# Optimization experiments

Hardware: AMD Instinct MI355X
Metric: run time of the kernel (lower is better)

The kernel has to match this reference:

```python
import jax, jax.numpy as jnp
import numpy as np

NUM_EMBEDDINGS = 512
EMBEDDING_DIM = 128
COMMITMENT_COST = 0.6
MID_HR = 100.0
HR_RANGE = 70.0


def setup_inputs() -> dict:
    key = jax.random.key(0)
    k1, k2 = jax.random.split(key)
    inputs = jax.random.normal(k1, (64, 2048, EMBEDDING_DIM), dtype=jnp.float32)
    # torch init: uniform(-1/K, 1/K)
    emb_weight = jax.random.uniform(
        k2, (NUM_EMBEDDINGS, EMBEDDING_DIM), dtype=jnp.float32,
        minval=-1.0 / NUM_EMBEDDINGS, maxval=1.0 / NUM_EMBEDDINGS)
    scaling = jnp.ones((NUM_EMBEDDINGS,), dtype=jnp.float32)
    return {"inputs": inputs, "emb_weight": emb_weight, "scaling": scaling}


def reference(inputs, emb_weight, scaling):
    B, T, D = inputs.shape
    K = emb_weight.shape[0]
    flat = inputs.reshape(-1, D)  # [N, D]
    # squared L2 distances to all codes: [N, K]
    distances = (
        jnp.sum(flat * flat, axis=1, keepdims=True)
        + jnp.sum(emb_weight * emb_weight, axis=1)
        - 2.0 * flat @ emb_weight.T
    )
    hr_values = jnp.linspace(40.0, 180.0, K, dtype=jnp.float32)
    hr_weights = 1.0 + scaling * ((hr_values - MID_HR) / HR_RANGE)  # [K]
    encoding_indices = jnp.argmin(distances * hr_weights[None, :], axis=1)  # [N]
    # one-hot @ codebook == direct gather
    quantized = emb_weight[encoding_indices].reshape(inputs.shape)
    e_latent_loss = jnp.mean((jax.lax.stop_gradient(quantized) - inputs) ** 2)
    q_latent_loss = jnp.mean((quantized - jax.lax.stop_gradient(inputs)) ** 2)
    loss = q_latent_loss + COMMITMENT_COST * e_latent_loss
    # straight-through estimator
    quantized_st = inputs + jax.lax.stop_gradient(quantized - inputs)
    return quantized_st, loss, encoding_indices.reshape(B, T)
```

## Files before the change

kernel.cpp:

```cpp
#include <hip/hip_runtime.h>

#define NCODES 512
#define DIM 128
#define NROWS (64*2048)
#define QN (NROWS*DIM)
#define BLK_ROWS 256
#define NBLOCKS (NROWS/BLK_ROWS)
#define NWAVES 8

typedef __attribute__((ext_vector_type(4))) float f32x4;

#define GLOAD_LDS16(gp, lp) __builtin_amdgcn_global_load_lds( \
    (__attribute__((address_space(1))) void*)(gp), \
    (__attribute__((address_space(3))) void*)(lp), 16, 0, 0)

__global__ void vq_prep(const float* __restrict__ emb, const float* __restrict__ scaling,
                        unsigned char* __restrict__ e8frag,
                        float* __restrict__ wv, float* __restrict__ wse,
                        float* __restrict__ wrcp) {
  int k = blockIdx.x;
  int l = threadIdx.x;
  float2 v = ((const float2*)(emb + k * DIM))[l];
  float ss = v.x * v.x + v.y * v.y;
#pragma unroll
  for (int m = 1; m < 64; m <<= 1) ss += __shfl_xor(ss, m);
  int p = __builtin_amdgcn_cvt_pk_fp8_f32(v.x * 512.0f, v.y * 512.0f, 0, false);
  int t = k >> 4, col = k & 15;
  int c = l >> 4, g = (l >> 2) & 3, jp = l & 3;
  *(unsigned short*)(e8frag + (((t * 4 + c) * 64 + g * 16 + col) << 3) + 2 * jp) =
      (unsigned short)(p & 0xFFFF);
  if (l == 0) {
    float hr = 40.0f + (float)k * (140.0f / 511.0f);
    float wt = 1.0f + scaling[k] * ((hr - 100.0f) * (1.0f / 70.0f));
    wv[k] = wt;
    wse[k] = wt * ss;
    wrcp[k] = 1.0f / wt;
  }
}

struct SmemT {
  unsigned char frag[NCODES * DIM];
  float w[NCODES];
  float wse[NCODES];
  float wrcp[NCODES];
  float lossp[NWAVES];
};

__global__ __launch_bounds__(512, 4) void vq_main(
    const float* __restrict__ x,
    const float* __restrict__ emb32,
    const unsigned char* __restrict__ e8frag,
    const float* __restrict__ wv,
    const float* __restrict__ wse,
    const float* __restrict__ wrcp,
    float* __restrict__ out_q,
    float* __restrict__ out_idx,
    float* __restrict__ out_loss) {
  __shared__ SmemT sm;
  const int tid = threadIdx.x;
  const int wave = tid >> 6, lane = tid & 63;
  const int g = lane >> 4, lr = lane & 15;
  const long rowbase = (long)blockIdx.x * BLK_ROWS + wave * 32;

  float4 xv[2][4][2];
#pragma unroll
  for (int rg = 0; rg < 2; rg++) {
    const float* xr = x + (rowbase + rg * 16 + lr) * DIM + g * 8;
#pragma unroll
    for (int c = 0; c < 4; c++) {
      xv[rg][c][0] = *(const float4*)(xr + c * 32);
      xv[rg][c][1] = *(const float4*)(xr + c * 32 + 4);
    }
  }

  {
#pragma unroll
    for (int i = 0; i < 8; i++) {
      int slot = i * 512 + tid;
      GLOAD_LDS16(e8frag + slot * 16, sm.frag + slot * 16);
    }
    sm.w[tid] = wv[tid]; sm.wse[tid] = wse[tid]; sm.wrcp[tid] = wrcp[tid];
    int t2 = tid + 512 - 512; (void)t2;
  }

  long a[2][4];
  float sr[2][4];
  {
    float srow[2];
#pragma unroll
    for (int rg = 0; rg < 2; rg++) {
      float ss = 0.f;
#pragma unroll
      for (int c = 0; c < 4; c++) {
        float4 v0 = xv[rg][c][0];
        float4 v1 = xv[rg][c][1];
        ss += v0.x * v0.x + v0.y * v0.y + v0.z * v0.z + v0.w * v0.w;
        ss += v1.x * v1.x + v1.y * v1.y + v1.z * v1.z + v1.w * v1.w;
        int lo = __builtin_amdgcn_cvt_pk_fp8_f32(v0.x, v0.y, 0, false);
        lo = __builtin_amdgcn_cvt_pk_fp8_f32(v0.z, v0.w, lo, true);
        int hi = __builtin_amdgcn_cvt_pk_fp8_f32(v1.x, v1.y, 0, false);
        hi = __builtin_amdgcn_cvt_pk_fp8_f32(v1.z, v1.w, hi, true);
        a[rg][c] = (long)(((unsigned long long)(unsigned)hi << 32) |
                          (unsigned long long)(unsigned)lo);
      }
      ss += __shfl_xor(ss, 16);
      ss += __shfl_xor(ss, 32);
      srow[rg] = ss;
    }
#pragma unroll
    for (int rg = 0; rg < 2; rg++)
#pragma unroll
      for (int r = 0; r < 4; r++)
        sr[rg][r] = __shfl(srow[rg], g * 4 + r);
  }
  __syncthreads();

  unsigned pmin[2][4];
#pragma unroll
  for (int rg = 0; rg < 2; rg++)
#pragma unroll
    for (int r = 0; r < 4; r++) pmin[rg][r] = 0xFFFFFFFFu;

  const long* __restrict__ bbase = (const long*)sm.frag + lane;
#pragma unroll 2
  for (int t = 0; t < 32; t++) {
    const unsigned code = t * 16 + lr;
    const float wt = sm.w[code];
    const float bb = sm.wse[code];
    const float m2w = -2.0f * wt * (1.0f / 512.0f);
    f32x4 acc0 = {0.f, 0.f, 0.f, 0.f};
    f32x4 acc1 = {0.f, 0.f, 0.f, 0.f};
#pragma unroll
    for (int c = 0; c < 4; c++) {
      long bf = bbase[(t * 4 + c) * 64];
      acc0 = __builtin_amdgcn_mfma_f32_16x16x32_fp8_fp8(a[0][c], bf, acc0, 0, 0, 0);
      acc1 = __builtin_amdgcn_mfma_f32_16x16x32_fp8_fp8(a[1][c], bf, acc1, 0, 0, 0);
    }
#pragma unroll
    for (int r = 0; r < 4; r++) {
      float v0 = fmaf(m2w, acc0[r], fmaf(wt, sr[0][r], bb));
      float v1 = fmaf(m2w, acc1[r], fmaf(wt, sr[1][r], bb));
      unsigned u0 = (__builtin_bit_cast(unsigned, v0) & 0xFFFFFE00u) | code;
      unsigned u1 = (__builtin_bit_cast(unsigned, v1) & 0xFFFFFE00u) | code;
      pmin[0][r] = min(pmin[0][r], u0);
      pmin[1][r] = min(pmin[1][r], u1);
    }
  }

#pragma unroll
  for (int m = 1; m <= 8; m <<= 1) {
#pragma unroll
    for (int rg = 0; rg < 2; rg++)
#pragma unroll
      for (int r = 0; r < 4; r++) {
        unsigned o = (unsigned)__shfl_xor((int)pmin[rg][r], m);
        pmin[rg][r] = min(pmin[rg][r], o);
      }
  }

  const uint4* __restrict__ esrc = (const uint4*)emb32;
  uint4* __restrict__ outu = (uint4*)out_q + rowbase * 32;
  const int col = lane & 31;
  const int hi2 = lane >> 5;
  int scode[16];
#pragma unroll
  for (int it = 0; it < 16; it++) {
    const int row0 = 2 * it;
    const int rg = row0 >> 4;
    const int gn = (row0 >> 2) & 3;
    const int r0 = row0 & 3;
    int c0 = __shfl((int)pmin[rg][r0], gn * 16);
    int c1 = __shfl((int)pmin[rg][r0 + 1], gn * 16);
    scode[it] = (hi2 ? c1 : c0) & 511;
  }

  uint4 vbuf[8];
#pragma unroll
  for (int j = 0; j < 8; j++)
    vbuf[j] = esrc[scode[j] * 32 + col];

  {
    float l0 = 0.f;
#pragma unroll
    for (int rg = 0; rg < 2; rg++)
#pragma unroll
      for (int r = 0; r < 4; r++) {
        unsigned wn = pmin[rg][r];
        int ci = (int)(wn & 511u);
        float dist = __builtin_bit_cast(float, wn & 0xFFFFFE00u);
        l0 = fmaf(dist, sm.wrcp[ci], l0);
        if (lr == 0) out_idx[rowbase + rg * 16 + g * 4 + r] = (float)ci;
      }
    l0 += __shfl_xor(l0, 16);
    l0 += __shfl_xor(l0, 32);
    if (lane == 0) sm.lossp[wave] = l0;
  }

#pragma unroll
  for (int j = 0; j < 8; j++)
    outu[j * 64 + lane] = vbuf[j];
#pragma unroll
  for (int j = 0; j < 8; j++)
    vbuf[j] = esrc[scode[8 + j] * 32 + col];
#pragma unroll
  for (int j = 0; j < 8; j++)
    outu[(8 + j) * 64 + lane] = vbuf[j];

  __syncthreads();
  if (wave == 0 && lane < NWAVES) {
    float s = sm.lossp[lane];
#pragma unroll
    for (int m = 1; m < NWAVES; m <<= 1) s += __shfl_xor(s, m);
    if (lane == 0) atomicAdd(out_loss, s * (1.6f / (float)QN));
  }
}

extern "C" void kernel_launch(void* const* d_in, const int* in_sizes, int n_in,
                              void* d_out, int out_size, void* d_ws, size_t ws_size,
                              hipStream_t stream) {
  const float* x = (const float*)d_in[0];
  const float* emb = (const float*)d_in[1];
  const float* scaling = (const float*)d_in[2];

  float* out_q = (float*)d_out;
  float* out_loss = out_q + QN;
  float* out_idx = out_q + QN + 1;

  unsigned char* e8frag = (unsigned char*)d_ws;
  float* wv = (float*)((char*)d_ws + NCODES * DIM);
  float* wse = wv + NCODES;
  float* wrcp = wse + NCODES;

  hipMemsetAsync(out_loss, 0, sizeof(float), stream);
  vq_prep<<<NCODES, 64, 0, stream>>>(emb, scaling, e8frag, wv, wse, wrcp);
  vq_main<<<NBLOCKS, 512, 0, stream>>>(x, emb, e8frag, wv, wse, wrcp,
                                       out_q, out_idx, out_loss);
}
```

Before: 43.02 us.

## Halve rows per block: one 16-row MFMA tile per wave instead of two

```diff
diff --git a/kernel.cpp b/kernel.cpp
--- a/kernel.cpp
+++ b/kernel.cpp
@@ -4,7 +4,7 @@
 #define DIM 128
 #define NROWS (64*2048)
 #define QN (NROWS*DIM)
-#define BLK_ROWS 256
+#define BLK_ROWS 128
 #define NBLOCKS (NROWS/BLK_ROWS)
 #define NWAVES 8
 
@@ -60,16 +60,15 @@
   const int tid = threadIdx.x;
   const int wave = tid >> 6, lane = tid & 63;
   const int g = lane >> 4, lr = lane & 15;
-  const long rowbase = (long)blockIdx.x * BLK_ROWS + wave * 32;
-
-  float4 xv[2][4][2];
-#pragma unroll
-  for (int rg = 0; rg < 2; rg++) {
-    const float* xr = x + (rowbase + rg * 16 + lr) * DIM + g * 8;
+  const long rowbase = (long)blockIdx.x * BLK_ROWS + wave * 16;
+
+  float4 xv[4][2];
+  {
+    const float* xr = x + (rowbase + lr) * DIM + g * 8;
 #pragma unroll
     for (int c = 0; c < 4; c++) {
-      xv[rg][c][0] = *(const float4*)(xr + c * 32);
-      xv[rg][c][1] = *(const float4*)(xr + c * 32 + 4);
+      xv[c][0] = *(const float4*)(xr + c * 32);
+      xv[c][1] = *(const float4*)(xr + c * 32 + 4);
     }
   }
 
@@ -80,46 +79,36 @@
       GLOAD_LDS16(e8frag + slot * 16, sm.frag + slot * 16);
     }
     sm.w[tid] = wv[tid]; sm.wse[tid] = wse[tid]; sm.wrcp[tid] = wrcp[tid];
-    int t2 = tid + 512 - 512; (void)t2;
-  }
-
-  long a[2][4];
-  float sr[2][4];
-  {
-    float srow[2];
-#pragma unroll
-    for (int rg = 0; rg < 2; rg++) {
-      float ss = 0.f;
-#pragma unroll
-      for (int c = 0; c < 4; c++) {
-        float4 v0 = xv[rg][c][0];
-        float4 v1 = xv[rg][c][1];
-        ss += v0.x * v0.x + v0.y * v0.y + v0.z * v0.z + v0.w * v0.w;
-        ss += v1.x * v1.x + v1.y * v1.y + v1.z * v1.z + v1.w * v1.w;
-        int lo = __builtin_amdgcn_cvt_pk_fp8_f32(v0.x, v0.y, 0, false);
-        lo = __builtin_amdgcn_cvt_pk_fp8_f32(v0.z, v0.w, lo, true);
-        int hi = __builtin_amdgcn_cvt_pk_fp8_f32(v1.x, v1.y, 0, false);
-        hi = __builtin_amdgcn_cvt_pk_fp8_f32(v1.z, v1.w, hi, true);
-        a[rg][c] = (long)(((unsigned long long)(unsigned)hi << 32) |
-                          (unsigned long long)(unsigned)lo);
-      }
-      ss += __shfl_xor(ss, 16);
-      ss += __shfl_xor(ss, 32);
-      srow[rg] = ss;
-    }
-#pragma unroll
-    for (int rg = 0; rg < 2; rg++)
-#pragma unroll
-      for (int r = 0; r < 4; r++)
-        sr[rg][r] = __shfl(srow[rg], g * 4 + r);
+  }
+
+  long a[4];
+  float sr[4];
+  {
+    float ss = 0.f;
+#pragma unroll
+    for (int c = 0; c < 4; c++) {
+      float4 v0 = xv[c][0];
+      float4 v1 = xv[c][1];
+      ss += v0.x * v0.x + v0.y * v0.y + v0.z * v0.z + v0.w * v0.w;
+      ss += v1.x * v1.x + v1.y * v1.y + v1.z * v1.z + v1.w * v1.w;
+      int lo = __builtin_amdgcn_cvt_pk_fp8_f32(v0.x, v0.y, 0, false);
+      lo = __builtin_amdgcn_cvt_pk_fp8_f32(v0.z, v0.w, lo, true);
+      int hi = __builtin_amdgcn_cvt_pk_fp8_f32(v1.x, v1.y, 0, false);
+      hi = __builtin_amdgcn_cvt_pk_fp8_f32(v1.z, v1.w, hi, true);
+      a[c] = (long)(((unsigned long long)(unsigned)hi << 32) |
+                    (unsigned long long)(unsigned)lo);
+    }
+    ss += __shfl_xor(ss, 16);
+    ss += __shfl_xor(ss, 32);
+#pragma unroll
+    for (int r = 0; r < 4; r++)
+      sr[r] = __shfl(ss, g * 4 + r);
   }
   __syncthreads();
 
-  unsigned pmin[2][4];
-#pragma unroll
-  for (int rg = 0; rg < 2; rg++)
-#pragma unroll
-    for (int r = 0; r < 4; r++) pmin[rg][r] = 0xFFFFFFFFu;
+  unsigned pmin[4];
+#pragma unroll
+  for (int r = 0; r < 4; r++) pmin[r] = 0xFFFFFFFFu;
 
   const long* __restrict__ bbase = (const long*)sm.frag + lane;
 #pragma unroll 2
@@ -128,49 +117,39 @@
     const float wt = sm.w[code];
     const float bb = sm.wse[code];
     const float m2w = -2.0f * wt * (1.0f / 512.0f);
-    f32x4 acc0 = {0.f, 0.f, 0.f, 0.f};
-    f32x4 acc1 = {0.f, 0.f, 0.f, 0.f};
+    f32x4 acc = {0.f, 0.f, 0.f, 0.f};
 #pragma unroll
     for (int c = 0; c < 4; c++) {
       long bf = bbase[(t * 4 + c) * 64];
-      acc0 = __builtin_amdgcn_mfma_f32_16x16x32_fp8_fp8(a[0][c], bf, acc0, 0, 0, 0);
-      acc1 = __builtin_amdgcn_mfma_f32_16x16x32_fp8_fp8(a[1][c], bf, acc1, 0, 0, 0);
+      acc = __builtin_amdgcn_mfma_f32_16x16x32_fp8_fp8(a[c], bf, acc, 0, 0, 0);
     }
 #pragma unroll
     for (int r = 0; r < 4; r++) {
-      float v0 = fmaf(m2w, acc0[r], fmaf(wt, sr[0][r], bb));
-      float v1 = fmaf(m2w, acc1[r], fmaf(wt, sr[1][r], bb));
-      unsigned u0 = (__builtin_bit_cast(unsigned, v0) & 0xFFFFFE00u) | code;
-      unsigned u1 = (__builtin_bit_cast(unsigned, v1) & 0xFFFFFE00u) | code;
-      pmin[0][r] = min(pmin[0][r], u0);
-      pmin[1][r] = min(pmin[1][r], u1);
+      float v = fmaf(m2w, acc[r], fmaf(wt, sr[r], bb));
+      unsigned u = (__builtin_bit_cast(unsigned, v) & 0xFFFFFE00u) | code;
+      pmin[r] = min(pmin[r], u);
     }
   }
 
 #pragma unroll
   for (int m = 1; m <= 8; m <<= 1) {
 #pragma unroll
-    for (int rg = 0; rg < 2; rg++)
-#pragma unroll
-      for (int r = 0; r < 4; r++) {
-        unsigned o = (unsigned)__shfl_xor((int)pmin[rg][r], m);
-        pmin[rg][r] = min(pmin[rg][r], o);
-      }
+    for (int r = 0; r < 4; r++) {
+      unsigned o = (unsigned)__shfl_xor((int)pmin[r], m);
+      pmin[r] = min(pmin[r], o);
+    }
   }
 
   const uint4* __restrict__ esrc = (const uint4*)emb32;
   uint4* __restrict__ outu = (uint4*)out_q + rowbase * 32;
   const int col = lane & 31;
   const int hi2 = lane >> 5;
-  int scode[16];
-#pragma unroll
-  for (int it = 0; it < 16; it++) {
+  int scode[8];
+#pragma unroll
+  for (int it = 0; it < 8; it++) {
     const int row0 = 2 * it;
-    const int rg = row0 >> 4;
-    const int gn = (row0 >> 2) & 3;
-    const int r0 = row0 & 3;
-    int c0 = __shfl((int)pmin[rg][r0], gn * 16);
-    int c1 = __shfl((int)pmin[rg][r0 + 1], gn * 16);
+    int c0 = __shfl((int)pmin[row0 & 3], (row0 >> 2) * 16);
+    int c1 = __shfl((int)pmin[(row0 + 1) & 3], ((row0 + 1) >> 2) * 16);
     scode[it] = (hi2 ? c1 : c0) & 511;
   }
 
@@ -182,15 +161,13 @@
   {
     float l0 = 0.f;
 #pragma unroll
-    for (int rg = 0; rg < 2; rg++)
-#pragma unroll
-      for (int r = 0; r < 4; r++) {
-        unsigned wn = pmin[rg][r];
-        int ci = (int)(wn & 511u);
-        float dist = __builtin_bit_cast(float, wn & 0xFFFFFE00u);
-        l0 = fmaf(dist, sm.wrcp[ci], l0);
-        if (lr == 0) out_idx[rowbase + rg * 16 + g * 4 + r] = (float)ci;
-      }
+    for (int r = 0; r < 4; r++) {
+      unsigned wn = pmin[r];
+      int ci = (int)(wn & 511u);
+      float dist = __builtin_bit_cast(float, wn & 0xFFFFFE00u);
+      l0 = fmaf(dist, sm.wrcp[ci], l0);
+      if (lr == 0) out_idx[rowbase + g * 4 + r] = (float)ci;
+    }
     l0 += __shfl_xor(l0, 16);
     l0 += __shfl_xor(l0, 32);
     if (lane == 0) sm.lossp[wave] = l0;
@@ -199,12 +176,6 @@
 #pragma unroll
   for (int j = 0; j < 8; j++)
     outu[j * 64 + lane] = vbuf[j];
-#pragma unroll
-  for (int j = 0; j < 8; j++)
-    vbuf[j] = esrc[scode[8 + j] * 32 + col];
-#pragma unroll
-  for (int j = 0; j < 8; j++)
-    outu[(8 + j) * 64 + lane] = vbuf[j];
 
   __syncthreads();
   if (wave == 0 && lane < NWAVES) {
```

Measured after the change: 44.75 us. 1.04x slower.

## Replace FP8 MFMA distance search with norm-bound pruning and exact fallback

Applied to the files above, without the earlier changes.

```diff
diff --git a/kernel.cpp b/kernel.cpp
--- a/kernel.cpp
+++ b/kernel.cpp
@@ -8,51 +8,40 @@
 #define NBLOCKS (NROWS/BLK_ROWS)
 #define NWAVES 8
 
-typedef __attribute__((ext_vector_type(4))) float f32x4;
-
-#define GLOAD_LDS16(gp, lp) __builtin_amdgcn_global_load_lds( \
-    (__attribute__((address_space(1))) void*)(gp), \
-    (__attribute__((address_space(3))) void*)(lp), 16, 0, 0)
-
 __global__ void vq_prep(const float* __restrict__ emb, const float* __restrict__ scaling,
-                        unsigned char* __restrict__ e8frag,
-                        float* __restrict__ wv, float* __restrict__ wse,
-                        float* __restrict__ wrcp) {
+                        float* __restrict__ wv, float* __restrict__ ssv,
+                        float* __restrict__ betav, float* __restrict__ gammav) {
   int k = blockIdx.x;
   int l = threadIdx.x;
   float2 v = ((const float2*)(emb + k * DIM))[l];
   float ss = v.x * v.x + v.y * v.y;
 #pragma unroll
   for (int m = 1; m < 64; m <<= 1) ss += __shfl_xor(ss, m);
-  int p = __builtin_amdgcn_cvt_pk_fp8_f32(v.x * 512.0f, v.y * 512.0f, 0, false);
-  int t = k >> 4, col = k & 15;
-  int c = l >> 4, g = (l >> 2) & 3, jp = l & 3;
-  *(unsigned short*)(e8frag + (((t * 4 + c) * 64 + g * 16 + col) << 3) + 2 * jp) =
-      (unsigned short)(p & 0xFFFF);
   if (l == 0) {
     float hr = 40.0f + (float)k * (140.0f / 511.0f);
     float wt = 1.0f + scaling[k] * ((hr - 100.0f) * (1.0f / 70.0f));
     wv[k] = wt;
-    wse[k] = wt * ss;
-    wrcp[k] = 1.0f / wt;
+    ssv[k] = ss;
+    betav[k] = wt * ss;
+    gammav[k] = 2.0f * fabsf(wt) * sqrtf(ss) * (1.0f + 1e-5f);
   }
 }
 
 struct SmemT {
-  unsigned char frag[NCODES * DIM];
   float w[NCODES];
-  float wse[NCODES];
-  float wrcp[NCODES];
+  float ss[NCODES];
+  float beta[NCODES];
+  float gamma[NCODES];
   float lossp[NWAVES];
 };
 
 __global__ __launch_bounds__(512, 4) void vq_main(
     const float* __restrict__ x,
     const float* __restrict__ emb32,
-    const unsigned char* __restrict__ e8frag,
     const float* __restrict__ wv,
-    const float* __restrict__ wse,
-    const float* __restrict__ wrcp,
+    const float* __restrict__ ssv,
+    const float* __restrict__ betav,
+    const float* __restrict__ gammav,
     float* __restrict__ out_q,
     float* __restrict__ out_idx,
     float* __restrict__ out_loss) {
@@ -62,6 +51,11 @@
   const int g = lane >> 4, lr = lane & 15;
   const long rowbase = (long)blockIdx.x * BLK_ROWS + wave * 32;
 
+  sm.w[tid] = wv[tid];
+  sm.ss[tid] = ssv[tid];
+  sm.beta[tid] = betav[tid];
+  sm.gamma[tid] = gammav[tid];
+
   float4 xv[2][4][2];
 #pragma unroll
   for (int rg = 0; rg < 2; rg++) {
@@ -72,139 +66,151 @@
       xv[rg][c][1] = *(const float4*)(xr + c * 32 + 4);
     }
   }
-
+  float srow[2], xn[2];
+#pragma unroll
+  for (int rg = 0; rg < 2; rg++) {
+    float ss = 0.f;
+#pragma unroll
+    for (int c = 0; c < 4; c++) {
+      float4 v0 = xv[rg][c][0];
+      float4 v1 = xv[rg][c][1];
+      ss += v0.x * v0.x + v0.y * v0.y + v0.z * v0.z + v0.w * v0.w;
+      ss += v1.x * v1.x + v1.y * v1.y + v1.z * v1.z + v1.w * v1.w;
+    }
+    ss += __shfl_xor(ss, 16);
+    ss += __shfl_xor(ss, 32);
+    srow[rg] = ss;
+    xn[rg] = sqrtf(ss);
+  }
+  __syncthreads();
+
+  int kb[2];
+#pragma unroll
+  for (int rg = 0; rg < 2; rg++) {
+    float fmin = 3.4e38f;
+    int imin = 0;
+#pragma unroll 8
+    for (int j = 0; j < 128; j++) {
+      int k = g * 128 + j;
+      float L = fmaf(-sm.gamma[k], xn[rg], fmaf(sm.w[k], srow[rg], sm.beta[k]));
+      if (L < fmin) { fmin = L; imin = k; }
+    }
+#pragma unroll
+    for (int m = 16; m <= 32; m <<= 1) {
+      float of = __shfl_xor(fmin, m);
+      int oi = __shfl_xor(imin, m);
+      if (of < fmin || (of == fmin && oi < imin)) { fmin = of; imin = oi; }
+    }
+    kb[rg] = imin;
+  }
+
+  int win[2];
+  float Drow[2], dWv[2];
+#pragma unroll
+  for (int rg = 0; rg < 2; rg++) {
+    const int k = kb[rg];
+    const float* er = emb32 + k * DIM + g * 8;
+    float p = 0.f;
+#pragma unroll
+    for (int c = 0; c < 4; c++) {
+      float4 e0 = *(const float4*)(er + c * 32);
+      float4 e1 = *(const float4*)(er + c * 32 + 4);
+      float4 a0 = xv[rg][c][0], a1 = xv[rg][c][1];
+      p = fmaf(a0.x, e0.x, p); p = fmaf(a0.y, e0.y, p);
+      p = fmaf(a0.z, e0.z, p); p = fmaf(a0.w, e0.w, p);
+      p = fmaf(a1.x, e1.x, p); p = fmaf(a1.y, e1.y, p);
+      p = fmaf(a1.z, e1.z, p); p = fmaf(a1.w, e1.w, p);
+    }
+    p += __shfl_xor(p, 16);
+    p += __shfl_xor(p, 32);
+    float D = srow[rg] + sm.ss[k] - 2.0f * p;
+    win[rg] = k;
+    Drow[rg] = D;
+    dWv[rg] = sm.w[k] * D;
+  }
+
+  int extra = 0;
+#pragma unroll
+  for (int rg = 0; rg < 2; rg++) {
+    float thr = dWv[rg] + fabsf(dWv[rg]) * 1e-6f;
+#pragma unroll 8
+    for (int j = 0; j < 128; j++) {
+      int k = g * 128 + j;
+      float L = fmaf(-sm.gamma[k], xn[rg], fmaf(sm.w[k], srow[rg], sm.beta[k]));
+      extra |= (L <= thr) & (k != kb[rg]);
+    }
+  }
+  if (__any(extra)) {
+#pragma unroll
+    for (int rg = 0; rg < 2; rg++) {
+      float bd = 3.4e38f, bD = 0.f;
+      int bi = 0;
+      for (int k = 0; k < NCODES; k++) {
+        const float* er = emb32 + k * DIM + g * 8;
+        float p = 0.f;
+#pragma unroll
+        for (int c = 0; c < 4; c++) {
+          float4 e0 = *(const float4*)(er + c * 32);
+          float4 e1 = *(const float4*)(er + c * 32 + 4);
+          float4 a0 = xv[rg][c][0], a1 = xv[rg][c][1];
+          p = fmaf(a0.x, e0.x, p); p = fmaf(a0.y, e0.y, p);
+          p = fmaf(a0.z, e0.z, p); p = fmaf(a0.w, e0.w, p);
+          p = fmaf(a1.x, e1.x, p); p = fmaf(a1.y, e1.y, p);
+          p = fmaf(a1.z, e1.z, p); p = fmaf(a1.w, e1.w, p);
+        }
+        p += __shfl_xor(p, 16);
+        p += __shfl_xor(p, 32);
+        float D = srow[rg] + sm.ss[k] - 2.0f * p;
+        float dw = sm.w[k] * D;
+        if (dw < bd) { bd = dw; bi = k; bD = D; }
+      }
+      win[rg] = bi;
+      Drow[rg] = bD;
+    }
+  }
+
+  if (g == 0) {
+    out_idx[rowbase + lr] = (float)win[0];
+    out_idx[rowbase + 16 + lr] = (float)win[1];
+  }
   {
-#pragma unroll
-    for (int i = 0; i < 8; i++) {
-      int slot = i * 512 + tid;
-      GLOAD_LDS16(e8frag + slot * 16, sm.frag + slot * 16);
-    }
-    sm.w[tid] = wv[tid]; sm.wse[tid] = wse[tid]; sm.wrcp[tid] = wrcp[tid];
-    int t2 = tid + 512 - 512; (void)t2;
-  }
-
-  long a[2][4];
-  float sr[2][4];
+    float l0 = Drow[0] + Drow[1];
+    l0 += __shfl_xor(l0, 1);
+    l0 += __shfl_xor(l0, 2);
+    l0 += __shfl_xor(l0, 4);
+    l0 += __shfl_xor(l0, 8);
+    if (lane == 0) sm.lossp[wave] = l0;
+  }
+
   {
-    float srow[2];
-#pragma unroll
-    for (int rg = 0; rg < 2; rg++) {
-      float ss = 0.f;
-#pragma unroll
-      for (int c = 0; c < 4; c++) {
-        float4 v0 = xv[rg][c][0];
-        float4 v1 = xv[rg][c][1];
-        ss += v0.x * v0.x + v0.y * v0.y + v0.z * v0.z + v0.w * v0.w;
-        ss += v1.x * v1.x + v1.y * v1.y + v1.z * v1.z + v1.w * v1.w;
-        int lo = __builtin_amdgcn_cvt_pk_fp8_f32(v0.x, v0.y, 0, false);
-        lo = __builtin_amdgcn_cvt_pk_fp8_f32(v0.z, v0.w, lo, true);
-        int hi = __builtin_amdgcn_cvt_pk_fp8_f32(v1.x, v1.y, 0, false);
-        hi = __builtin_amdgcn_cvt_pk_fp8_f32(v1.z, v1.w, hi, true);
-        a[rg][c] = (long)(((unsigned long long)(unsigned)hi << 32) |
-                          (unsigned long long)(unsigned)lo);
-      }
-      ss += __shfl_xor(ss, 16);
-      ss += __shfl_xor(ss, 32);
-      srow[rg] = ss;
-    }
-#pragma unroll
-    for (int rg = 0; rg < 2; rg++)
-#pragma unroll
-      for (int r = 0; r < 4; r++)
-        sr[rg][r] = __shfl(srow[rg], g * 4 + r);
-  }
-  __syncthreads();
-
-  unsigned pmin[2][4];
-#pragma unroll
-  for (int rg = 0; rg < 2; rg++)
-#pragma unroll
-    for (int r = 0; r < 4; r++) pmin[rg][r] = 0xFFFFFFFFu;
-
-  const long* __restrict__ bbase = (const long*)sm.frag + lane;
-#pragma unroll 2
-  for (int t = 0; t < 32; t++) {
-    const unsigned code = t * 16 + lr;
-    const float wt = sm.w[code];
-    const float bb = sm.wse[code];
-    const float m2w = -2.0f * wt * (1.0f / 512.0f);
-    f32x4 acc0 = {0.f, 0.f, 0.f, 0.f};
-    f32x4 acc1 = {0.f, 0.f, 0.f, 0.f};
-#pragma unroll
-    for (int c = 0; c < 4; c++) {
-      long bf = bbase[(t * 4 + c) * 64];
-      acc0 = __builtin_amdgcn_mfma_f32_16x16x32_fp8_fp8(a[0][c], bf, acc0, 0, 0, 0);
-      acc1 = __builtin_amdgcn_mfma_f32_16x16x32_fp8_fp8(a[1][c], bf, acc1, 0, 0, 0);
-    }
-#pragma unroll
-    for (int r = 0; r < 4; r++) {
-      float v0 = fmaf(m2w, acc0[r], fmaf(wt, sr[0][r], bb));
-      float v1 = fmaf(m2w, acc1[r], fmaf(wt, sr[1][r], bb));
-      unsigned u0 = (__builtin_bit_cast(unsigned, v0) & 0xFFFFFE00u) | code;
-      unsigned u1 = (__builtin_bit_cast(unsigned, v1) & 0xFFFFFE00u) | code;
-      pmin[0][r] = min(pmin[0][r], u0);
-      pmin[1][r] = min(pmin[1][r], u1);
-    }
-  }
-
-#pragma unroll
-  for (int m = 1; m <= 8; m <<= 1) {
-#pragma unroll
-    for (int rg = 0; rg < 2; rg++)
-#pragma unroll
-      for (int r = 0; r < 4; r++) {
-        unsigned o = (unsigned)__shfl_xor((int)pmin[rg][r], m);
-        pmin[rg][r] = min(pmin[rg][r], o);
-      }
-  }
-
-  const uint4* __restrict__ esrc = (const uint4*)emb32;
-  uint4* __restrict__ outu = (uint4*)out_q + rowbase * 32;
-  const int col = lane & 31;
-  const int hi2 = lane >> 5;
-  int scode[16];
-#pragma unroll
-  for (int it = 0; it < 16; it++) {
-    const int row0 = 2 * it;
-    const int rg = row0 >> 4;
-    const int gn = (row0 >> 2) & 3;
-    const int r0 = row0 & 3;
-    int c0 = __shfl((int)pmin[rg][r0], gn * 16);
-    int c1 = __shfl((int)pmin[rg][r0 + 1], gn * 16);
-    scode[it] = (hi2 ? c1 : c0) & 511;
-  }
-
-  uint4 vbuf[8];
-#pragma unroll
-  for (int j = 0; j < 8; j++)
-    vbuf[j] = esrc[scode[j] * 32 + col];
-
-  {
-    float l0 = 0.f;
-#pragma unroll
-    for (int rg = 0; rg < 2; rg++)
-#pragma unroll
-      for (int r = 0; r < 4; r++) {
-        unsigned wn = pmin[rg][r];
-        int ci = (int)(wn & 511u);
-        float dist = __builtin_bit_cast(float, wn & 0xFFFFFE00u);
-        l0 = fmaf(dist, sm.wrcp[ci], l0);
-        if (lr == 0) out_idx[rowbase + rg * 16 + g * 4 + r] = (float)ci;
-      }
-    l0 += __shfl_xor(l0, 16);
-    l0 += __shfl_xor(l0, 32);
-    if (lane == 0) sm.lossp[wave] = l0;
-  }
-
-#pragma unroll
-  for (int j = 0; j < 8; j++)
-    outu[j * 64 + lane] = vbuf[j];
-#pragma unroll
-  for (int j = 0; j < 8; j++)
-    vbuf[j] = esrc[scode[8 + j] * 32 + col];
-#pragma unroll
-  for (int j = 0; j < 8; j++)
-    outu[(8 + j) * 64 + lane] = vbuf[j];
+    const uint4* __restrict__ esrc = (const uint4*)emb32;
+    uint4* __restrict__ outu = (uint4*)out_q + rowbase * 32;
+    const int col = lane & 31;
+    const int hi2 = lane >> 5;
+    int scode[16];
+#pragma unroll
+    for (int it = 0; it < 16; it++) {
+      const int row0 = 2 * it;
+      const int rg = row0 >> 4;
+      const int m = row0 & 15;
+      int c0 = __shfl(win[rg], m);
+      int c1 = __shfl(win[rg], m + 1);
+      scode[it] = hi2 ? c1 : c0;
+    }
+    uint4 vbuf[8];
+#pragma unroll
+    for (int j = 0; j < 8; j++)
+      vbuf[j] = esrc[scode[j] * 32 + col];
+#pragma unroll
+    for (int j = 0; j < 8; j++)
+      outu[j * 64 + lane] = vbuf[j];
+#pragma unroll
+    for (int j = 0; j < 8; j++)
+      vbuf[j] = esrc[scode[8 + j] * 32 + col];
+#pragma unroll
+    for (int j = 0; j < 8; j++)
+      outu[(8 + j) * 64 + lane] = vbuf[j];
+  }
 
   __syncthreads();
   if (wave == 0 && lane < NWAVES) {
@@ -226,13 +232,13 @@
   float* out_loss = out_q + QN;
   float* out_idx = out_q + QN + 1;
 
-  unsigned char* e8frag = (unsigned char*)d_ws;
-  float* wv = (float*)((char*)d_ws + NCODES * DIM);
-  float* wse = wv + NCODES;
-  float* wrcp = wse + NCODES;
+  float* wv = (float*)d_ws;
+  float* ssv = wv + NCODES;
+  float* betav = ssv + NCODES;
+  float* gammav = betav + NCODES;
 
   hipMemsetAsync(out_loss, 0, sizeof(float), stream);
-  vq_prep<<<NCODES, 64, 0, stream>>>(emb, scaling, e8frag, wv, wse, wrcp);
-  vq_main<<<NBLOCKS, 512, 0, stream>>>(x, emb, e8frag, wv, wse, wrcp,
+  vq_prep<<<NCODES, 64, 0, stream>>>(emb, scaling, wv, ssv, betav, gammav);
+  vq_main<<<NBLOCKS, 512, 0, stream>>>(x, emb, wv, ssv, betav, gammav,
                                        out_q, out_idx, out_loss);
 }
```

Measured after the change: 79.17 us. +84.0%, slower.
